# Optimization experiments

Measured on AMD Instinct MI355X. Metric: run time of the kernel, lower is better.

The kernel has to match this reference:

```python
import jax, jax.numpy as jnp
import numpy as np

B, At, Nbr = 4, 1024, 32
Fn, Fe, L = 128, 128, 3
N_TYPES = 100
G_END = 5.5  # gaussian_filter_end = cutoff - 0.5
ZIN = 2 * Fn + Fe


def setup_inputs() -> dict:
    key = jax.random.key(0)
    ks = jax.random.split(key, 16)
    s = lambda fan: 1.0 / np.sqrt(fan)
    inp = {}
    inp["Z"] = jax.random.randint(ks[0], (B, At), 0, N_TYPES)
    inp["nbr_idx"] = jax.random.randint(ks[1], (B, At, Nbr), 0, At)
    inp["distances"] = jax.random.uniform(ks[2], (B, At, Nbr), jnp.float32) * 6.0
    inp["unit_vecs"] = jax.random.normal(ks[3], (B, At, Nbr, 3), jnp.float32)
    # learned parameters
    inp["emb_table"] = jax.random.normal(ks[4], (N_TYPES, Fn), jnp.float32)
    inp["Wnf"] = jax.random.normal(ks[5], (L, ZIN, Fn), jnp.float32) * s(ZIN)
    inp["bnf"] = jnp.zeros((L, Fn), jnp.float32)
    inp["Wnc"] = jax.random.normal(ks[6], (L, ZIN, Fn), jnp.float32) * s(ZIN)
    inp["bnc"] = jnp.zeros((L, Fn), jnp.float32)
    inp["Wef"] = jax.random.normal(ks[7], (L, ZIN, Fe), jnp.float32) * s(ZIN)
    inp["bef"] = jnp.zeros((L, Fe), jnp.float32)
    inp["Wec"] = jax.random.normal(ks[8], (L, ZIN, Fe), jnp.float32) * s(ZIN)
    inp["bec"] = jnp.zeros((L, Fe), jnp.float32)
    # ForceMagnitudeMapping: 2 output layers, softplus on hidden, none on last
    inp["Wo1"] = jax.random.normal(ks[9], (Fe, Fe // 2), jnp.float32) * s(Fe)
    inp["bo1"] = jnp.zeros((Fe // 2,), jnp.float32)
    inp["Wo2"] = jax.random.normal(ks[10], (Fe // 2, 1), jnp.float32) * s(Fe // 2)
    inp["bo2"] = jnp.zeros((1,), jnp.float32)
    return inp


def _gather_nbr(h, nbr_idx):
    # h: [B, At, F], nbr_idx: [B, At, Nbr] -> [B, At, Nbr, F]
    b, at, f = h.shape
    nbr = nbr_idx.shape[-1]
    idx = nbr_idx.reshape(b, at * nbr, 1)
    return jnp.take_along_axis(h, idx, axis=1).reshape(b, at, nbr, f)


def reference(Z, nbr_idx, distances, unit_vecs, emb_table,
              Wnf, bnf, Wnc, bnc, Wef, bef, Wec, bec,
              Wo1, bo1, Wo2, bo2):
    # Gaussian filter of neighbor distances -> initial edge embedding [B,At,Nbr,Fe]
    mu = jnp.linspace(0.0, G_END, Fe)
    coeff = -0.5 / (mu[1] - mu[0]) ** 2
    e = jnp.exp(coeff * (distances[..., None] - mu) ** 2)
    # node embedding lookup [B,At,Fn]
    h = emb_table[Z]
    for l in range(L):
        # node update: gated (CGCNN-style) aggregation over neighbor edges
        hj = _gather_nbr(h, nbr_idx)
        hi = jnp.broadcast_to(h[:, :, None, :], hj.shape)
        z = jnp.concatenate([hi, hj, e], axis=-1)  # [B,At,Nbr,2Fn+Fe]
        msg = jax.nn.sigmoid(z @ Wnf[l] + bnf[l]) * jax.nn.softplus(z @ Wnc[l] + bnc[l])
        h = h + msg.sum(axis=2)
        # edge update from the freshly updated endpoint node features
        hj2 = _gather_nbr(h, nbr_idx)
        hi2 = jnp.broadcast_to(h[:, :, None, :], hj2.shape)
        z2 = jnp.concatenate([hi2, hj2, e], axis=-1)
        e = e + jax.nn.sigmoid(z2 @ Wef[l] + bef[l]) * jax.nn.softplus(z2 @ Wec[l] + bec[l])
    # force-magnitude mapping: softplus hidden, linear last -> [B,At,Nbr,1]
    fm = jax.nn.softplus(e @ Wo1 + bo1) @ Wo2 + bo2
    # expand over xyz, weight by unit vectors, reduce over neighbors
    forces = (fm * unit_vecs).sum(axis=2)  # [B,At,3]
    return forces
```

## Files before the change

kernel.cpp:

```cpp
#include <hip/hip_runtime.h>
#include <math.h>

#define AT 1024
#define NBR 32
#define FN 128
#define FE 128
#define ZIN 384
#define NA 4096
#define NEDGE (NA * NBR)
#define WSTRIDE (ZIN * FN)
#define G_ENDF 5.5f
#define WTMAT (384 * 128)
#define EPART (256 * 128)

typedef unsigned short ushort_t;
typedef __attribute__((ext_vector_type(8))) short bf16x8;
typedef __attribute__((ext_vector_type(4))) float f32x4;

#define LOG2E 1.4426950408889634f
#define LN2   0.6931471805599453f

__device__ __forceinline__ float fexp(float x) {
    return __builtin_amdgcn_exp2f(x * LOG2E);
}
__device__ __forceinline__ float sigmoid_f(float x) {
    return __builtin_amdgcn_rcpf(1.0f + __builtin_amdgcn_exp2f(-x * LOG2E));
}
__device__ __forceinline__ float softplus_f(float x) {
    float t = __builtin_amdgcn_exp2f(-fabsf(x) * LOG2E);
    return fmaxf(x, 0.0f) + LN2 * __builtin_amdgcn_logf(1.0f + t);
}

__device__ __forceinline__ ushort_t f2bf(float f) {
    unsigned int u = __float_as_uint(f);
    u = (u + 0x7FFFu + ((u >> 16) & 1u)) >> 16;
    return (ushort_t)u;
}
__device__ __forceinline__ float bf2f(ushort_t h) {
    return __uint_as_float(((unsigned int)h) << 16);
}
__device__ __forceinline__ unsigned int cvt_pk_bf16(float a, float b) {
    unsigned int r;
    asm("v_cvt_pk_bf16_f32 %0, %1, %2" : "=v"(r) : "v"(a), "v"(b));
    return r;
}
__device__ __forceinline__ void split2(float a, float b,
                                       unsigned int& hi, unsigned int& lo) {
    hi = cvt_pk_bf16(a, b);
    float ha = __uint_as_float(hi << 16);
    float hb = __uint_as_float(hi & 0xffff0000u);
    lo = cvt_pk_bf16(a - ha, b - hb);
}

__global__ __launch_bounds__(256) void k_init_h(const int* __restrict__ Z,
                                                const float* __restrict__ emb,
                                                float* __restrict__ h) {
    int idx = blockIdx.x * 256 + threadIdx.x;
    int atom = idx >> 7, f = idx & 127;
    h[idx] = emb[Z[atom] * FN + f];
}

__global__ __launch_bounds__(256) void k_conv_w(const float* __restrict__ Wnf,
                                                const float* __restrict__ Wnc,
                                                const float* __restrict__ Wef,
                                                const float* __restrict__ Wec,
                                                ushort_t* __restrict__ Whi,
                                                ushort_t* __restrict__ Wlo) {
    const int blk = blockIdx.x;
    const int w = blk / 3, p = blk % 3;
    const int l = w >> 2, t = w & 3;
    const float* src = (t == 0 ? Wnf : t == 1 ? Wnc : t == 2 ? Wef : Wec)
                       + (size_t)l * WSTRIDE + (size_t)p * 128 * 128;
    __shared__ float tile[128][129];
    const int tid = threadIdx.x;
    {
        int k = tid >> 1, h = (tid & 1) * 64;
#pragma unroll
        for (int i = 0; i < 16; ++i) {
            float4 v = *(const float4*)&src[k * 128 + h + i * 4];
            tile[k][h + i * 4 + 0] = v.x; tile[k][h + i * 4 + 1] = v.y;
            tile[k][h + i * 4 + 2] = v.z; tile[k][h + i * 4 + 3] = v.w;
        }
    }
    __syncthreads();
    {
        int f = tid >> 1, kh = (tid & 1) * 64;
        size_t orow = (size_t)(w * 384 + p * 128 + f) * 128;
#pragma unroll
        for (int i = 0; i < 64; i += 4) {
            ushort4 ph, pl;
            float x0 = tile[kh + i + 0][f]; ph.x = f2bf(x0); pl.x = f2bf(x0 - bf2f(ph.x));
            float x1 = tile[kh + i + 1][f]; ph.y = f2bf(x1); pl.y = f2bf(x1 - bf2f(ph.y));
            float x2 = tile[kh + i + 2][f]; ph.z = f2bf(x2); pl.z = f2bf(x2 - bf2f(ph.z));
            float x3 = tile[kh + i + 3][f]; ph.w = f2bf(x3); pl.w = f2bf(x3 - bf2f(ph.w));
            *(ushort4*)&Whi[orow + kh + i] = ph;
            *(ushort4*)&Wlo[orow + kh + i] = pl;
        }
    }
}

__global__ __launch_bounds__(256) void k_conv_wo(const float* __restrict__ Wo1,
                                                 ushort_t* __restrict__ Wh,
                                                 ushort_t* __restrict__ Wl) {
    int idx = blockIdx.x * 256 + threadIdx.x;
    int n = idx >> 7, k = idx & 127;
    float x = Wo1[k * 64 + n];
    ushort_t h = f2bf(x);
    Wh[idx] = h;
    Wl[idx] = f2bf(x - bf2f(h));
}

__global__ __launch_bounds__(512, 4) void k_proj(
    const float* __restrict__ h,
    const ushort_t* __restrict__ Wah, const ushort_t* __restrict__ Wal,
    const ushort_t* __restrict__ Wbh, const ushort_t* __restrict__ Wbl,
    const float* __restrict__ ba, const float* __restrict__ bb,
    float* __restrict__ Pi, float* __restrict__ Pj) {
    const int tid = threadIdx.x;
    const int a0 = blockIdx.x * 16;
    __shared__ __align__(16) ushort_t sAh[16 * 136];
    __shared__ __align__(16) ushort_t sAl[16 * 136];
    {
        int row = tid >> 5, kq = (tid & 31) * 4;
        float4 v = *(const float4*)&h[(size_t)(a0 + row) * 128 + kq];
        unsigned int h0, l0, h1, l1;
        split2(v.x, v.y, h0, l0);
        split2(v.z, v.w, h1, l1);
        *(uint2*)&sAh[row * 136 + kq] = make_uint2(h0, h1);
        *(uint2*)&sAl[row * 136 + kq] = make_uint2(l0, l1);
    }
    __syncthreads();

    const int w = tid >> 6;
    const int lane = tid & 63;
    const int lrow = lane & 15;
    const int kgrp = (lane >> 4) * 8;

    f32x4 acc[4] = {};
#pragma unroll
    for (int kk = 0; kk < 4; ++kk) {
        const int kbase = kk * 32 + kgrp;
        bf16x8 ah = *(const bf16x8*)&sAh[lrow * 136 + kbase];
        bf16x8 al = *(const bf16x8*)&sAl[lrow * 136 + kbase];
#pragma unroll
        for (int nt = 0; nt < 4; ++nt) {
            int r512 = w * 64 + nt * 16 + lrow;
            const ushort_t* bh_p = (r512 < 256) ? (Wah + (size_t)r512 * 128)
                                                : (Wbh + (size_t)(r512 - 256) * 128);
            const ushort_t* bl_p = (r512 < 256) ? (Wal + (size_t)r512 * 128)
                                                : (Wbl + (size_t)(r512 - 256) * 128);
            bf16x8 bh = *(const bf16x8*)&bh_p[kbase];
            bf16x8 bl = *(const bf16x8*)&bl_p[kbase];
            acc[nt] = __builtin_amdgcn_mfma_f32_16x16x32_bf16(ah, bh, acc[nt], 0, 0, 0);
            acc[nt] = __builtin_amdgcn_mfma_f32_16x16x32_bf16(ah, bl, acc[nt], 0, 0, 0);
            acc[nt] = __builtin_amdgcn_mfma_f32_16x16x32_bf16(al, bh, acc[nt], 0, 0, 0);
        }
    }

    const int arr = w >> 1;
    float* dst = (arr & 1) ? Pj : Pi;
    const int slot = arr >> 1;
    const int rb = (lane >> 4) * 4;
#pragma unroll
    for (int nt = 0; nt < 4; ++nt) {
        int f = (w & 1) * 64 + nt * 16 + lrow;
        float bs = (arr == 0) ? ba[f] : (arr == 2) ? bb[f] : 0.0f;
#pragma unroll
        for (int r = 0; r < 4; ++r) {
            int row = rb + r;
            dst[((size_t)(a0 + row) * 128 + f) * 2 + slot] = acc[nt][r] + bs;
        }
    }
}

template <int NODE, int FIRST, int FUSE>
__global__ __launch_bounds__(512, 4) void k_pass(
    const float* __restrict__ e_g, float* __restrict__ e_out,
    const float* __restrict__ dist, const int* __restrict__ nbr,
    const float* __restrict__ Pi, const float* __restrict__ Pj,
    const ushort_t* __restrict__ Wfh, const ushort_t* __restrict__ Wfl,
    const ushort_t* __restrict__ Wch, const ushort_t* __restrict__ Wcl,
    const float* __restrict__ h_old, float* __restrict__ h_new,
    const ushort_t* __restrict__ Wo1h, const ushort_t* __restrict__ Wo1l,
    const float* __restrict__ bo1, const float* __restrict__ Wo2,
    const float* __restrict__ bo2, const float* __restrict__ unit,
    float* __restrict__ out) {
    const int tid = threadIdx.x;
    const int a0 = blockIdx.x * 2;
    const int base = (a0 >> 10) << 10;

    __shared__ __align__(16) ushort_t sAh[64 * 136];
    __shared__ __align__(16) ushort_t sAl[64 * 136];
    __shared__ int snbr[64];
    __shared__ float sred[4][64];

    {
        int row = tid >> 3, kq = (tid & 7) * 16;
        size_t eoff = ((size_t)(a0 * 32 + row)) * 128 + kq;
        float v[16];
        if (FIRST) {
            const float delta = G_ENDF / 127.0f;
            const float coeff = -0.5f / (delta * delta);
            float d = dist[a0 * 32 + row];
#pragma unroll
            for (int i = 0; i < 16; ++i) {
                float x = d - (float)(kq + i) * delta;
                v[i] = fexp(coeff * x * x);
            }
#pragma unroll
            for (int i = 0; i < 4; ++i)
                *(float4*)&e_out[eoff + i * 4] =
                    make_float4(v[i * 4], v[i * 4 + 1], v[i * 4 + 2], v[i * 4 + 3]);
        } else {
#pragma unroll
            for (int i = 0; i < 4; ++i) {
                float4 t = *(const float4*)&e_g[eoff + i * 4];
                v[i * 4] = t.x; v[i * 4 + 1] = t.y; v[i * 4 + 2] = t.z; v[i * 4 + 3] = t.w;
            }
        }
#pragma unroll
        for (int i = 0; i < 4; ++i) {
            unsigned int h0, l0, h1, l1;
            split2(v[i * 4 + 0], v[i * 4 + 1], h0, l0);
            split2(v[i * 4 + 2], v[i * 4 + 3], h1, l1);
            *(uint2*)&sAh[row * 136 + kq + i * 4] = make_uint2(h0, h1);
            *(uint2*)&sAl[row * 136 + kq + i * 4] = make_uint2(l0, l1);
        }
    }
    if (tid < 64) snbr[tid] = nbr[a0 * 32 + tid];
    __syncthreads();

    const int w = tid >> 6;
    const int lane = tid & 63;
    const int wr = w >> 2;
    const int wc = w & 3;
    const int lrow = lane & 15;
    const int kgrp = (lane >> 4) * 8;
    const int rb = (lane >> 4) * 4;

    float2 pi_[2];
    float2 pj_[2][8];
#pragma unroll
    for (int nt = 0; nt < 2; ++nt) {
        const int nn = wc * 32 + nt * 16 + lrow;
        pi_[nt] = *(const float2*)&Pi[((size_t)(a0 + wr) * 128 + nn) * 2];
#pragma unroll
        for (int mt = 0; mt < 2; ++mt)
#pragma unroll
            for (int r = 0; r < 4; ++r) {
                const int rl = wr * 32 + mt * 16 + rb + r;
                const int j = base + snbr[rl];
                pj_[nt][mt * 4 + r] = *(const float2*)&Pj[((size_t)j * 128 + nn) * 2];
            }
    }

    f32x4 accf[2][2] = {};
    f32x4 accc[2][2] = {};

#pragma unroll
    for (int kk = 0; kk < 4; ++kk) {
        const int kbase = kk * 32 + kgrp;
        bf16x8 ah[2], al[2];
#pragma unroll
        for (int mt = 0; mt < 2; ++mt) {
            ah[mt] = *(const bf16x8*)&sAh[(wr * 32 + mt * 16 + lrow) * 136 + kbase];
            al[mt] = *(const bf16x8*)&sAl[(wr * 32 + mt * 16 + lrow) * 136 + kbase];
        }
#pragma unroll
        for (int nt = 0; nt < 2; ++nt) {
            const int nn = wc * 32 + nt * 16 + lrow;
            bf16x8 bfh = *(const bf16x8*)&Wfh[(size_t)nn * 128 + kbase];
            bf16x8 bfl = *(const bf16x8*)&Wfl[(size_t)nn * 128 + kbase];
            bf16x8 bch = *(const bf16x8*)&Wch[(size_t)nn * 128 + kbase];
            bf16x8 bcl = *(const bf16x8*)&Wcl[(size_t)nn * 128 + kbase];
#pragma unroll
            for (int mt = 0; mt < 2; ++mt) {
                accf[mt][nt] = __builtin_amdgcn_mfma_f32_16x16x32_bf16(ah[mt], bfh, accf[mt][nt], 0, 0, 0);
                accf[mt][nt] = __builtin_amdgcn_mfma_f32_16x16x32_bf16(ah[mt], bfl, accf[mt][nt], 0, 0, 0);
                accf[mt][nt] = __builtin_amdgcn_mfma_f32_16x16x32_bf16(al[mt], bfh, accf[mt][nt], 0, 0, 0);
                accc[mt][nt] = __builtin_amdgcn_mfma_f32_16x16x32_bf16(ah[mt], bch, accc[mt][nt], 0, 0, 0);
                accc[mt][nt] = __builtin_amdgcn_mfma_f32_16x16x32_bf16(ah[mt], bcl, accc[mt][nt], 0, 0, 0);
                accc[mt][nt] = __builtin_amdgcn_mfma_f32_16x16x32_bf16(al[mt], bch, accc[mt][nt], 0, 0, 0);
            }
        }
    }

    if (FUSE) __syncthreads();

    float hsum[2] = {0.0f, 0.0f};
#pragma unroll
    for (int nt = 0; nt < 2; ++nt) {
        const int nn = wc * 32 + nt * 16 + lrow;
#pragma unroll
        for (int mt = 0; mt < 2; ++mt) {
#pragma unroll
            for (int r = 0; r < 4; ++r) {
                const int rl = wr * 32 + mt * 16 + rb + r;
                const int idx = mt * 4 + r;
                float cf = accf[mt][nt][r] + pi_[nt].x + pj_[nt][idx].x;
                float cc = accc[mt][nt][r] + pi_[nt].y + pj_[nt][idx].y;
                float msg = sigmoid_f(cf) * softplus_f(cc);
                if (NODE) {
                    hsum[nt] += msg;
                } else {
                    const int lidx = rl * 136 + nn;
                    float eold = bf2f(sAh[lidx]) + bf2f(sAl[lidx]);
                    float enew = eold + msg;
                    if (FUSE) {
                        ushort_t hh = f2bf(enew);
                        sAh[lidx] = hh;
                        sAl[lidx] = f2bf(enew - bf2f(hh));
                    } else {
                        e_out[((size_t)(a0 * 32 + rl)) * 128 + nn] = enew;
                    }
                }
            }
        }
    }

    if (NODE) {
#pragma unroll
        for (int nt = 0; nt < 2; ++nt) {
            float v = hsum[nt];
            v += __shfl_xor(v, 16, 64);
            v += __shfl_xor(v, 32, 64);
            if (lane < 16) {
                int col = wc * 32 + nt * 16 + lane;
                h_new[(size_t)(a0 + wr) * 128 + col] =
                    h_old[(size_t)(a0 + wr) * 128 + col] + v;
            }
        }
    }

    if (FUSE) {
        __syncthreads();
        f32x4 acco[2] = {};
        const int col = wc * 16 + lrow;
#pragma unroll
        for (int kk = 0; kk < 4; ++kk) {
            const int kbase = kk * 32 + kgrp;
            bf16x8 bh = *(const bf16x8*)&Wo1h[(size_t)col * 128 + kbase];
            bf16x8 bl = *(const bf16x8*)&Wo1l[(size_t)col * 128 + kbase];
#pragma unroll
            for (int mt = 0; mt < 2; ++mt) {
                bf16x8 ah = *(const bf16x8*)&sAh[(wr * 32 + mt * 16 + lrow) * 136 + kbase];
                bf16x8 al = *(const bf16x8*)&sAl[(wr * 32 + mt * 16 + lrow) * 136 + kbase];
                acco[mt] = __builtin_amdgcn_mfma_f32_16x16x32_bf16(ah, bh, acco[mt], 0, 0, 0);
                acco[mt] = __builtin_amdgcn_mfma_f32_16x16x32_bf16(ah, bl, acco[mt], 0, 0, 0);
                acco[mt] = __builtin_amdgcn_mfma_f32_16x16x32_bf16(al, bh, acco[mt], 0, 0, 0);
            }
        }
        const float b1 = bo1[col];
        const float w2 = Wo2[col];
#pragma unroll
        for (int mt = 0; mt < 2; ++mt) {
#pragma unroll
            for (int r = 0; r < 4; ++r) {
                float val = softplus_f(acco[mt][r] + b1) * w2;
                val += __shfl_xor(val, 1, 64);
                val += __shfl_xor(val, 2, 64);
                val += __shfl_xor(val, 4, 64);
                val += __shfl_xor(val, 8, 64);
                if (lrow == 0) sred[wc][wr * 32 + mt * 16 + rb + r] = val;
            }
        }
        __syncthreads();
        if (tid < 6) {
            int a = (tid < 3) ? 0 : 1;
            int c = tid - a * 3;
            float b2 = bo2[0];
            float s = 0.0f;
#pragma unroll 4
            for (int n = 0; n < 32; ++n) {
                int row = a * 32 + n;
                float fm = sred[0][row] + sred[1][row] + sred[2][row] + sred[3][row] + b2;
                s += fm * unit[((size_t)((a0 + a) * 32 + n)) * 3 + c];
            }
            out[(size_t)(a0 + a) * 3 + c] = s;
        }
    }
}

extern "C" void kernel_launch(void* const* d_in, const int* in_sizes, int n_in,
                              void* d_out, int out_size, void* d_ws, size_t ws_size,
                              hipStream_t stream) {
    const int*   Z    = (const int*)d_in[0];
    const int*   nbr  = (const int*)d_in[1];
    const float* dist = (const float*)d_in[2];
    const float* unit = (const float*)d_in[3];
    const float* emb  = (const float*)d_in[4];
    const float* Wnf  = (const float*)d_in[5];
    const float* bnf  = (const float*)d_in[6];
    const float* Wnc  = (const float*)d_in[7];
    const float* bnc  = (const float*)d_in[8];
    const float* Wef  = (const float*)d_in[9];
    const float* bef  = (const float*)d_in[10];
    const float* Wec  = (const float*)d_in[11];
    const float* bec  = (const float*)d_in[12];
    const float* Wo1  = (const float*)d_in[13];
    const float* bo1  = (const float*)d_in[14];
    const float* Wo2  = (const float*)d_in[15];
    const float* bo2  = (const float*)d_in[16];
    float* out = (float*)d_out;

    float* ws = (float*)d_ws;
    float* e   = ws;
    float* h0  = e + (size_t)NEDGE * FE;
    float* h1  = h0 + (size_t)NA * FN;
    float* Pi  = h1 + (size_t)NA * FN;
    float* Pj  = Pi + (size_t)NA * FN * 2;
    ushort_t* Whi  = (ushort_t*)(Pj + (size_t)NA * FN * 2);
    ushort_t* Wlo  = Whi + (size_t)12 * WTMAT;
    ushort_t* Wo1h = Wlo + (size_t)12 * WTMAT;
    ushort_t* Wo1l = Wo1h + (size_t)64 * 128;

    k_conv_w<<<36, 256, 0, stream>>>(Wnf, Wnc, Wef, Wec, Whi, Wlo);
    k_conv_wo<<<32, 256, 0, stream>>>(Wo1, Wo1h, Wo1l);
    k_init_h<<<(NA * FN) / 256, 256, 0, stream>>>(Z, emb, h0);

    float* hc = h0;
    float* hn = h1;
    for (int l = 0; l < 3; ++l) {
        const ushort_t* nf_h = Whi + (size_t)(l * 4 + 0) * WTMAT;
        const ushort_t* nf_l = Wlo + (size_t)(l * 4 + 0) * WTMAT;
        const ushort_t* nc_h = Whi + (size_t)(l * 4 + 1) * WTMAT;
        const ushort_t* nc_l = Wlo + (size_t)(l * 4 + 1) * WTMAT;
        const ushort_t* ef_h = Whi + (size_t)(l * 4 + 2) * WTMAT;
        const ushort_t* ef_l = Wlo + (size_t)(l * 4 + 2) * WTMAT;
        const ushort_t* ec_h = Whi + (size_t)(l * 4 + 3) * WTMAT;
        const ushort_t* ec_l = Wlo + (size_t)(l * 4 + 3) * WTMAT;

        k_proj<<<NA / 16, 512, 0, stream>>>(hc, nf_h, nf_l, nc_h, nc_l,
                                            bnf + l * FN, bnc + l * FN, Pi, Pj);
        if (l == 0)
            k_pass<1, 1, 0><<<NA / 2, 512, 0, stream>>>(
                e, e, dist, nbr, Pi, Pj,
                nf_h + EPART, nf_l + EPART, nc_h + EPART, nc_l + EPART,
                hc, hn, nullptr, nullptr, nullptr, nullptr, nullptr, nullptr, nullptr);
        else
            k_pass<1, 0, 0><<<NA / 2, 512, 0, stream>>>(
                e, e, dist, nbr, Pi, Pj,
                nf_h + EPART, nf_l + EPART, nc_h + EPART, nc_l + EPART,
                hc, hn, nullptr, nullptr, nullptr, nullptr, nullptr, nullptr, nullptr);

        k_proj<<<NA / 16, 512, 0, stream>>>(hn, ef_h, ef_l, ec_h, ec_l,
                                            bef + l * FN, bec + l * FN, Pi, Pj);
        if (l < 2)
            k_pass<0, 0, 0><<<NA / 2, 512, 0, stream>>>(
                e, e, dist, nbr, Pi, Pj,
                ef_h + EPART, ef_l + EPART, ec_h + EPART, ec_l + EPART,
                nullptr, nullptr, nullptr, nullptr, nullptr, nullptr, nullptr, nullptr, nullptr);
        else
            k_pass<0, 0, 1><<<NA / 2, 512, 0, stream>>>(
                e, e, dist, nbr, Pi, Pj,
                ef_h + EPART, ef_l + EPART, ec_h + EPART, ec_l + EPART,
                nullptr, nullptr, Wo1h, Wo1l, bo1, Wo2, bo2, unit, out);

        float* t = hc; hc = hn; hn = t;
    }
}
```

Measured before the change: 672.3 us.

## Process four atom-pair tiles per block with double-buffered LDS prefetch

```diff
diff --git a/kernel.cpp b/kernel.cpp
--- a/kernel.cpp
+++ b/kernel.cpp
@@ -176,7 +176,7 @@
 template <int NODE, int FIRST, int FUSE>
 __global__ __launch_bounds__(512, 4) void k_pass(
     const float* __restrict__ e_g, float* __restrict__ e_out,
-    const float* __restrict__ dist, const int* __restrict__ nbr,
+    const float* __restrict__ dist, const int* __restrict__ nbr_g,
     const float* __restrict__ Pi, const float* __restrict__ Pj,
     const ushort_t* __restrict__ Wfh, const ushort_t* __restrict__ Wfl,
     const ushort_t* __restrict__ Wch, const ushort_t* __restrict__ Wcl,
@@ -186,49 +186,12 @@
     const float* __restrict__ bo2, const float* __restrict__ unit,
     float* __restrict__ out) {
     const int tid = threadIdx.x;
-    const int a0 = blockIdx.x * 2;
-    const int base = (a0 >> 10) << 10;
-
-    __shared__ __align__(16) ushort_t sAh[64 * 136];
-    __shared__ __align__(16) ushort_t sAl[64 * 136];
-    __shared__ int snbr[64];
+    const int ab = blockIdx.x * 8;
+    const int base = (ab >> 10) << 10;
+
+    __shared__ __align__(16) ushort_t sAh[2][64 * 136];
+    __shared__ __align__(16) ushort_t sAl[2][64 * 136];
     __shared__ float sred[4][64];
-
-    {
-        int row = tid >> 3, kq = (tid & 7) * 16;
-        size_t eoff = ((size_t)(a0 * 32 + row)) * 128 + kq;
-        float v[16];
-        if (FIRST) {
-            const float delta = G_ENDF / 127.0f;
-            const float coeff = -0.5f / (delta * delta);
-            float d = dist[a0 * 32 + row];
-#pragma unroll
-            for (int i = 0; i < 16; ++i) {
-                float x = d - (float)(kq + i) * delta;
-                v[i] = fexp(coeff * x * x);
-            }
-#pragma unroll
-            for (int i = 0; i < 4; ++i)
-                *(float4*)&e_out[eoff + i * 4] =
-                    make_float4(v[i * 4], v[i * 4 + 1], v[i * 4 + 2], v[i * 4 + 3]);
-        } else {
-#pragma unroll
-            for (int i = 0; i < 4; ++i) {
-                float4 t = *(const float4*)&e_g[eoff + i * 4];
-                v[i * 4] = t.x; v[i * 4 + 1] = t.y; v[i * 4 + 2] = t.z; v[i * 4 + 3] = t.w;
-            }
-        }
-#pragma unroll
-        for (int i = 0; i < 4; ++i) {
-            unsigned int h0, l0, h1, l1;
-            split2(v[i * 4 + 0], v[i * 4 + 1], h0, l0);
-            split2(v[i * 4 + 2], v[i * 4 + 3], h1, l1);
-            *(uint2*)&sAh[row * 136 + kq + i * 4] = make_uint2(h0, h1);
-            *(uint2*)&sAl[row * 136 + kq + i * 4] = make_uint2(l0, l1);
-        }
-    }
-    if (tid < 64) snbr[tid] = nbr[a0 * 32 + tid];
-    __syncthreads();
 
     const int w = tid >> 6;
     const int lane = tid & 63;
@@ -237,146 +200,225 @@
     const int lrow = lane & 15;
     const int kgrp = (lane >> 4) * 8;
     const int rb = (lane >> 4) * 4;
-
-    float2 pi_[2];
-    float2 pj_[2][8];
-#pragma unroll
-    for (int nt = 0; nt < 2; ++nt) {
-        const int nn = wc * 32 + nt * 16 + lrow;
-        pi_[nt] = *(const float2*)&Pi[((size_t)(a0 + wr) * 128 + nn) * 2];
-#pragma unroll
-        for (int mt = 0; mt < 2; ++mt)
-#pragma unroll
-            for (int r = 0; r < 4; ++r) {
-                const int rl = wr * 32 + mt * 16 + rb + r;
-                const int j = base + snbr[rl];
-                pj_[nt][mt * 4 + r] = *(const float2*)&Pj[((size_t)j * 128 + nn) * 2];
-            }
-    }
-
-    f32x4 accf[2][2] = {};
-    f32x4 accc[2][2] = {};
-
-#pragma unroll
-    for (int kk = 0; kk < 4; ++kk) {
-        const int kbase = kk * 32 + kgrp;
-        bf16x8 ah[2], al[2];
-#pragma unroll
-        for (int mt = 0; mt < 2; ++mt) {
-            ah[mt] = *(const bf16x8*)&sAh[(wr * 32 + mt * 16 + lrow) * 136 + kbase];
-            al[mt] = *(const bf16x8*)&sAl[(wr * 32 + mt * 16 + lrow) * 136 + kbase];
-        }
+    const int srow = tid >> 3;
+    const int skq = (tid & 7) * 16;
+
+    const float delta = G_ENDF / 127.0f;
+    const float coeff = -0.5f / (delta * delta);
+
+    float ev[16];
+    float dNext = 0.0f;
+    int nbrNext[8];
+    int nbrCur[8];
+
+    {
+        const int a0 = ab;
+        if (FIRST) {
+            dNext = dist[a0 * 32 + srow];
+        } else {
+            size_t eoff = ((size_t)(a0 * 32 + srow)) * 128 + skq;
+#pragma unroll
+            for (int i = 0; i < 4; ++i) *(float4*)&ev[i * 4] = *(const float4*)&e_g[eoff + i * 4];
+        }
+#pragma unroll
+        for (int i = 0; i < 8; ++i)
+            nbrNext[i] = nbr_g[(a0 + wr) * 32 + (i >> 2) * 16 + rb + (i & 3)];
+        if (FIRST) {
+#pragma unroll
+            for (int i = 0; i < 16; ++i) {
+                float x = dNext - (float)(skq + i) * delta;
+                ev[i] = fexp(coeff * x * x);
+            }
+            size_t eoff = ((size_t)(a0 * 32 + srow)) * 128 + skq;
+#pragma unroll
+            for (int i = 0; i < 4; ++i)
+                *(float4*)&e_out[eoff + i * 4] =
+                    make_float4(ev[i * 4], ev[i * 4 + 1], ev[i * 4 + 2], ev[i * 4 + 3]);
+        }
+#pragma unroll
+        for (int i = 0; i < 4; ++i) {
+            unsigned int h0, l0, h1, l1;
+            split2(ev[i * 4 + 0], ev[i * 4 + 1], h0, l0);
+            split2(ev[i * 4 + 2], ev[i * 4 + 3], h1, l1);
+            *(uint2*)&sAh[0][srow * 136 + skq + i * 4] = make_uint2(h0, h1);
+            *(uint2*)&sAl[0][srow * 136 + skq + i * 4] = make_uint2(l0, l1);
+        }
+#pragma unroll
+        for (int i = 0; i < 8; ++i) nbrCur[i] = nbrNext[i];
+    }
+    __syncthreads();
+
+#pragma unroll
+    for (int t = 0; t < 4; ++t) {
+        const int cur = t & 1;
+        const int a0 = ab + t * 2;
+
+        if (t < 3) {
+            const int a1 = a0 + 2;
+            if (FIRST) {
+                dNext = dist[a1 * 32 + srow];
+            } else {
+                size_t eoff = ((size_t)(a1 * 32 + srow)) * 128 + skq;
+#pragma unroll
+                for (int i = 0; i < 4; ++i) *(float4*)&ev[i * 4] = *(const float4*)&e_g[eoff + i * 4];
+            }
+#pragma unroll
+            for (int i = 0; i < 8; ++i)
+                nbrNext[i] = nbr_g[(a1 + wr) * 32 + (i >> 2) * 16 + rb + (i & 3)];
+        }
+        __builtin_amdgcn_sched_barrier(0);
+
+        f32x4 accf[2][2] = {};
+        f32x4 accc[2][2] = {};
+#pragma unroll
+        for (int kk = 0; kk < 4; ++kk) {
+            const int kbase = kk * 32 + kgrp;
+            bf16x8 ah[2], al[2];
+#pragma unroll
+            for (int mt = 0; mt < 2; ++mt) {
+                ah[mt] = *(const bf16x8*)&sAh[cur][(wr * 32 + mt * 16 + lrow) * 136 + kbase];
+                al[mt] = *(const bf16x8*)&sAl[cur][(wr * 32 + mt * 16 + lrow) * 136 + kbase];
+            }
+#pragma unroll
+            for (int nt = 0; nt < 2; ++nt) {
+                const int nn = wc * 32 + nt * 16 + lrow;
+                bf16x8 bfh = *(const bf16x8*)&Wfh[(size_t)nn * 128 + kbase];
+                bf16x8 bfl = *(const bf16x8*)&Wfl[(size_t)nn * 128 + kbase];
+                bf16x8 bch = *(const bf16x8*)&Wch[(size_t)nn * 128 + kbase];
+                bf16x8 bcl = *(const bf16x8*)&Wcl[(size_t)nn * 128 + kbase];
+#pragma unroll
+                for (int mt = 0; mt < 2; ++mt) {
+                    accf[mt][nt] = __builtin_amdgcn_mfma_f32_16x16x32_bf16(ah[mt], bfh, accf[mt][nt], 0, 0, 0);
+                    accf[mt][nt] = __builtin_amdgcn_mfma_f32_16x16x32_bf16(ah[mt], bfl, accf[mt][nt], 0, 0, 0);
+                    accf[mt][nt] = __builtin_amdgcn_mfma_f32_16x16x32_bf16(al[mt], bfh, accf[mt][nt], 0, 0, 0);
+                    accc[mt][nt] = __builtin_amdgcn_mfma_f32_16x16x32_bf16(ah[mt], bch, accc[mt][nt], 0, 0, 0);
+                    accc[mt][nt] = __builtin_amdgcn_mfma_f32_16x16x32_bf16(ah[mt], bcl, accc[mt][nt], 0, 0, 0);
+                    accc[mt][nt] = __builtin_amdgcn_mfma_f32_16x16x32_bf16(al[mt], bch, accc[mt][nt], 0, 0, 0);
+                }
+            }
+        }
+
+        if (FUSE) __syncthreads();
+
+        float hsum[2] = {0.0f, 0.0f};
 #pragma unroll
         for (int nt = 0; nt < 2; ++nt) {
             const int nn = wc * 32 + nt * 16 + lrow;
-            bf16x8 bfh = *(const bf16x8*)&Wfh[(size_t)nn * 128 + kbase];
-            bf16x8 bfl = *(const bf16x8*)&Wfl[(size_t)nn * 128 + kbase];
-            bf16x8 bch = *(const bf16x8*)&Wch[(size_t)nn * 128 + kbase];
-            bf16x8 bcl = *(const bf16x8*)&Wcl[(size_t)nn * 128 + kbase];
+            const float2 piv = *(const float2*)&Pi[((size_t)(a0 + wr) * 128 + nn) * 2];
 #pragma unroll
             for (int mt = 0; mt < 2; ++mt) {
-                accf[mt][nt] = __builtin_amdgcn_mfma_f32_16x16x32_bf16(ah[mt], bfh, accf[mt][nt], 0, 0, 0);
-                accf[mt][nt] = __builtin_amdgcn_mfma_f32_16x16x32_bf16(ah[mt], bfl, accf[mt][nt], 0, 0, 0);
-                accf[mt][nt] = __builtin_amdgcn_mfma_f32_16x16x32_bf16(al[mt], bfh, accf[mt][nt], 0, 0, 0);
-                accc[mt][nt] = __builtin_amdgcn_mfma_f32_16x16x32_bf16(ah[mt], bch, accc[mt][nt], 0, 0, 0);
-                accc[mt][nt] = __builtin_amdgcn_mfma_f32_16x16x32_bf16(ah[mt], bcl, accc[mt][nt], 0, 0, 0);
-                accc[mt][nt] = __builtin_amdgcn_mfma_f32_16x16x32_bf16(al[mt], bch, accc[mt][nt], 0, 0, 0);
-            }
-        }
-    }
-
-    if (FUSE) __syncthreads();
-
-    float hsum[2] = {0.0f, 0.0f};
-#pragma unroll
-    for (int nt = 0; nt < 2; ++nt) {
-        const int nn = wc * 32 + nt * 16 + lrow;
-#pragma unroll
-        for (int mt = 0; mt < 2; ++mt) {
-#pragma unroll
-            for (int r = 0; r < 4; ++r) {
-                const int rl = wr * 32 + mt * 16 + rb + r;
-                const int idx = mt * 4 + r;
-                float cf = accf[mt][nt][r] + pi_[nt].x + pj_[nt][idx].x;
-                float cc = accc[mt][nt][r] + pi_[nt].y + pj_[nt][idx].y;
-                float msg = sigmoid_f(cf) * softplus_f(cc);
-                if (NODE) {
-                    hsum[nt] += msg;
-                } else {
-                    const int lidx = rl * 136 + nn;
-                    float eold = bf2f(sAh[lidx]) + bf2f(sAl[lidx]);
-                    float enew = eold + msg;
-                    if (FUSE) {
-                        ushort_t hh = f2bf(enew);
-                        sAh[lidx] = hh;
-                        sAl[lidx] = f2bf(enew - bf2f(hh));
+#pragma unroll
+                for (int r = 0; r < 4; ++r) {
+                    const int rl = wr * 32 + mt * 16 + rb + r;
+                    const int j = base + nbrCur[mt * 4 + r];
+                    const float2 pjv = *(const float2*)&Pj[((size_t)j * 128 + nn) * 2];
+                    float cf = accf[mt][nt][r] + piv.x + pjv.x;
+                    float cc = accc[mt][nt][r] + piv.y + pjv.y;
+                    float msg = sigmoid_f(cf) * softplus_f(cc);
+                    if (NODE) {
+                        hsum[nt] += msg;
                     } else {
-                        e_out[((size_t)(a0 * 32 + rl)) * 128 + nn] = enew;
+                        const int lidx = rl * 136 + nn;
+                        float eold = bf2f(sAh[cur][lidx]) + bf2f(sAl[cur][lidx]);
+                        float enew = eold + msg;
+                        if (FUSE) {
+                            ushort_t hh = f2bf(enew);
+                            sAh[cur][lidx] = hh;
+                            sAl[cur][lidx] = f2bf(enew - bf2f(hh));
+                        } else {
+                            e_out[((size_t)(a0 * 32 + rl)) * 128 + nn] = enew;
+                        }
                     }
                 }
             }
         }
-    }
-
-    if (NODE) {
-#pragma unroll
-        for (int nt = 0; nt < 2; ++nt) {
-            float v = hsum[nt];
-            v += __shfl_xor(v, 16, 64);
-            v += __shfl_xor(v, 32, 64);
-            if (lane < 16) {
-                int col = wc * 32 + nt * 16 + lane;
-                h_new[(size_t)(a0 + wr) * 128 + col] =
-                    h_old[(size_t)(a0 + wr) * 128 + col] + v;
-            }
-        }
-    }
-
-    if (FUSE) {
+
+        if (NODE) {
+#pragma unroll
+            for (int nt = 0; nt < 2; ++nt) {
+                float v = hsum[nt];
+                v += __shfl_xor(v, 16, 64);
+                v += __shfl_xor(v, 32, 64);
+                if (lane < 16) {
+                    int col = wc * 32 + nt * 16 + lane;
+                    h_new[(size_t)(a0 + wr) * 128 + col] =
+                        h_old[(size_t)(a0 + wr) * 128 + col] + v;
+                }
+            }
+        }
+
+        if (t < 3) {
+            if (FIRST) {
+#pragma unroll
+                for (int i = 0; i < 16; ++i) {
+                    float x = dNext - (float)(skq + i) * delta;
+                    ev[i] = fexp(coeff * x * x);
+                }
+                size_t eoff = ((size_t)((a0 + 2) * 32 + srow)) * 128 + skq;
+#pragma unroll
+                for (int i = 0; i < 4; ++i)
+                    *(float4*)&e_out[eoff + i * 4] =
+                        make_float4(ev[i * 4], ev[i * 4 + 1], ev[i * 4 + 2], ev[i * 4 + 3]);
+            }
+#pragma unroll
+            for (int i = 0; i < 4; ++i) {
+                unsigned int h0, l0, h1, l1;
+                split2(ev[i * 4 + 0], ev[i * 4 + 1], h0, l0);
+                split2(ev[i * 4 + 2], ev[i * 4 + 3], h1, l1);
+                *(uint2*)&sAh[cur ^ 1][srow * 136 + skq + i * 4] = make_uint2(h0, h1);
+                *(uint2*)&sAl[cur ^ 1][srow * 136 + skq + i * 4] = make_uint2(l0, l1);
+            }
+#pragma unroll
+            for (int i = 0; i < 8; ++i) nbrCur[i] = nbrNext[i];
+        }
         __syncthreads();
-        f32x4 acco[2] = {};
-        const int col = wc * 16 + lrow;
-#pragma unroll
-        for (int kk = 0; kk < 4; ++kk) {
-            const int kbase = kk * 32 + kgrp;
-            bf16x8 bh = *(const bf16x8*)&Wo1h[(size_t)col * 128 + kbase];
-            bf16x8 bl = *(const bf16x8*)&Wo1l[(size_t)col * 128 + kbase];
+
+        if (FUSE) {
+            f32x4 acco[2] = {};
+            const int col = wc * 16 + lrow;
+#pragma unroll
+            for (int kk = 0; kk < 4; ++kk) {
+                const int kbase = kk * 32 + kgrp;
+                bf16x8 bh = *(const bf16x8*)&Wo1h[(size_t)col * 128 + kbase];
+                bf16x8 bl = *(const bf16x8*)&Wo1l[(size_t)col * 128 + kbase];
+#pragma unroll
+                for (int mt = 0; mt < 2; ++mt) {
+                    bf16x8 ah = *(const bf16x8*)&sAh[cur][(wr * 32 + mt * 16 + lrow) * 136 + kbase];
+                    bf16x8 al = *(const bf16x8*)&sAl[cur][(wr * 32 + mt * 16 + lrow) * 136 + kbase];
+                    acco[mt] = __builtin_amdgcn_mfma_f32_16x16x32_bf16(ah, bh, acco[mt], 0, 0, 0);
+                    acco[mt] = __builtin_amdgcn_mfma_f32_16x16x32_bf16(ah, bl, acco[mt], 0, 0, 0);
+                    acco[mt] = __builtin_amdgcn_mfma_f32_16x16x32_bf16(al, bh, acco[mt], 0, 0, 0);
+                }
+            }
+            const float b1 = bo1[col];
+            const float w2 = Wo2[col];
 #pragma unroll
             for (int mt = 0; mt < 2; ++mt) {
-                bf16x8 ah = *(const bf16x8*)&sAh[(wr * 32 + mt * 16 + lrow) * 136 + kbase];
-                bf16x8 al = *(const bf16x8*)&sAl[(wr * 32 + mt * 16 + lrow) * 136 + kbase];
-                acco[mt] = __builtin_amdgcn_mfma_f32_16x16x32_bf16(ah, bh, acco[mt], 0, 0, 0);
-                acco[mt] = __builtin_amdgcn_mfma_f32_16x16x32_bf16(ah, bl, acco[mt], 0, 0, 0);
-                acco[mt] = __builtin_amdgcn_mfma_f32_16x16x32_bf16(al, bh, acco[mt], 0, 0, 0);
-            }
-        }
-        const float b1 = bo1[col];
-        const float w2 = Wo2[col];
-#pragma unroll
-        for (int mt = 0; mt < 2; ++mt) {
-#pragma unroll
-            for (int r = 0; r < 4; ++r) {
-                float val = softplus_f(acco[mt][r] + b1) * w2;
-                val += __shfl_xor(val, 1, 64);
-                val += __shfl_xor(val, 2, 64);
-                val += __shfl_xor(val, 4, 64);
-                val += __shfl_xor(val, 8, 64);
-                if (lrow == 0) sred[wc][wr * 32 + mt * 16 + rb + r] = val;
-            }
-        }
-        __syncthreads();
-        if (tid < 6) {
-            int a = (tid < 3) ? 0 : 1;
-            int c = tid - a * 3;
-            float b2 = bo2[0];
-            float s = 0.0f;
+#pragma unroll
+                for (int r = 0; r < 4; ++r) {
+                    float val = softplus_f(acco[mt][r] + b1) * w2;
+                    val += __shfl_xor(val, 1, 64);
+                    val += __shfl_xor(val, 2, 64);
+                    val += __shfl_xor(val, 4, 64);
+                    val += __shfl_xor(val, 8, 64);
+                    if (lrow == 0) sred[wc][wr * 32 + mt * 16 + rb + r] = val;
+                }
+            }
+            __syncthreads();
+            if (tid < 6) {
+                int a = (tid < 3) ? 0 : 1;
+                int c = tid - a * 3;
+                float b2 = bo2[0];
+                float s = 0.0f;
 #pragma unroll 4
-            for (int n = 0; n < 32; ++n) {
-                int row = a * 32 + n;
-                float fm = sred[0][row] + sred[1][row] + sred[2][row] + sred[3][row] + b2;
-                s += fm * unit[((size_t)((a0 + a) * 32 + n)) * 3 + c];
-            }
-            out[(size_t)(a0 + a) * 3 + c] = s;
+                for (int n = 0; n < 32; ++n) {
+                    int row = a * 32 + n;
+                    float fm = sred[0][row] + sred[1][row] + sred[2][row] + sred[3][row] + b2;
+                    s += fm * unit[((size_t)((a0 + a) * 32 + n)) * 3 + c];
+                }
+                out[(size_t)(a0 + a) * 3 + c] = s;
+            }
+            __syncthreads();
         }
     }
 }
@@ -433,12 +475,12 @@
         k_proj<<<NA / 16, 512, 0, stream>>>(hc, nf_h, nf_l, nc_h, nc_l,
                                             bnf + l * FN, bnc + l * FN, Pi, Pj);
         if (l == 0)
-            k_pass<1, 1, 0><<<NA / 2, 512, 0, stream>>>(
+            k_pass<1, 1, 0><<<NA / 8, 512, 0, stream>>>(
                 e, e, dist, nbr, Pi, Pj,
                 nf_h + EPART, nf_l + EPART, nc_h + EPART, nc_l + EPART,
                 hc, hn, nullptr, nullptr, nullptr, nullptr, nullptr, nullptr, nullptr);
         else
-            k_pass<1, 0, 0><<<NA / 2, 512, 0, stream>>>(
+            k_pass<1, 0, 0><<<NA / 8, 512, 0, stream>>>(
                 e, e, dist, nbr, Pi, Pj,
                 nf_h + EPART, nf_l + EPART, nc_h + EPART, nc_l + EPART,
                 hc, hn, nullptr, nullptr, nullptr, nullptr, nullptr, nullptr, nullptr);
@@ -446,12 +488,12 @@
         k_proj<<<NA / 16, 512, 0, stream>>>(hn, ef_h, ef_l, ec_h, ec_l,
                                             bef + l * FN, bec + l * FN, Pi, Pj);
         if (l < 2)
-            k_pass<0, 0, 0><<<NA / 2, 512, 0, stream>>>(
+            k_pass<0, 0, 0><<<NA / 8, 512, 0, stream>>>(
                 e, e, dist, nbr, Pi, Pj,
                 ef_h + EPART, ef_l + EPART, ec_h + EPART, ec_l + EPART,
                 nullptr, nullptr, nullptr, nullptr, nullptr, nullptr, nullptr, nullptr, nullptr);
         else
-            k_pass<0, 0, 1><<<NA / 2, 512, 0, stream>>>(
+            k_pass<0, 0, 1><<<NA / 8, 512, 0, stream>>>(
                 e, e, dist, nbr, Pi, Pj,
                 ef_h + EPART, ef_l + EPART, ec_h + EPART, ec_l + EPART,
                 nullptr, nullptr, Wo1h, Wo1l, bo1, Wo2, bo2, unit, out);
```

Result: slower. 799.3 us (+18.9%).
